# Optimization experiments

Hardware: AMD Instinct MI355X
Metric: run time of the kernel (lower is better)

## Reference

```python
import jax, jax.numpy as jnp
import numpy as np

N_NODES = 50000
N_EDGES = 1600000
IN_CH, OUT_CH, SIZE = 128, 64, 4


def _segment_softmax(e, seg, n):
    # numerically stable softmax of edge scores grouped by segment id (PyG softmax)
    m = jax.ops.segment_max(e, seg, num_segments=n)
    ex = jnp.exp(e - m[seg])
    s = jax.ops.segment_sum(ex, seg, num_segments=n)
    return ex / (s[seg] + 1e-16)


def setup_inputs() -> dict:
    key = jax.random.key(0)
    k = jax.random.split(key, 6)
    x = jax.random.normal(k[0], (N_NODES, IN_CH), dtype=jnp.float32)
    edge_index = jax.random.randint(k[1], (2, N_EDGES), 0, N_NODES, dtype=jnp.int64)
    W = jax.random.normal(k[2], (SIZE, IN_CH, OUT_CH), dtype=jnp.float32) * 0.1
    att_src = jax.random.normal(k[3], (SIZE, OUT_CH), dtype=jnp.float32) * 0.1
    att_dst = jax.random.normal(k[4], (SIZE, OUT_CH), dtype=jnp.float32) * 0.1
    bias = jnp.zeros((SIZE, OUT_CH), dtype=jnp.float32)
    return {"x": x, "W": W, "att_src": att_src, "att_dst": att_dst,
            "bias": bias, "edge_index": edge_index, "direction": 1}


def reference(x, W, att_src, att_dst, bias, edge_index, direction):
    src, dst = edge_index[0], edge_index[1]
    n = x.shape[0]
    size = W.shape[0]
    feat_sum = None
    att_sum = None
    for i in range(size):  # small fixed ensemble of GATConv layers
        h = x @ W[i]                                    # [N, out]
        a_s = h @ att_src[i]                            # [N] source scores
        a_d = h @ att_dst[i]                            # [N] target scores
        e = jax.nn.leaky_relu(a_s[src] + a_d[dst], 0.2)  # [E] GAT slope 0.2
        alpha = _segment_softmax(e, dst, n)             # softmax over incoming edges
        out = jax.ops.segment_sum(alpha[:, None] * h[src], dst, num_segments=n) + bias[i]
        fl = jax.nn.leaky_relu(out, 0.01)               # f.leaky_relu default slope
        feat_sum = fl if feat_sum is None else feat_sum + fl
        att_sum = alpha if att_sum is None else att_sum + alpha
    # directional node pooling: mean of summed edge attention grouped by source node
    counts = jax.ops.segment_sum(jnp.ones_like(att_sum), src, num_segments=n)
    pooled = jax.ops.segment_sum(att_sum, src, num_segments=n) / jnp.maximum(counts, 1.0)
    node_scores = direction * pooled
    return feat_sum, node_scores
```

## Files before the change

kernel.cpp:

```cpp
#include <hip/hip_runtime.h>
#include <stdint.h>

#define N_NODES 50000
#define N_EDGES 1600000
#define IN_CH   128
#define OUT_CH  64
#define CAP     72
#define NBUCKET 196
#define MB      782
#define NODES48 (MB * 64)
#define GB      3128
#define EPB2    2047
#define BK2     24
#define GOVF_CAP 8192
#define NODES_PAD (NBUCKET * 256)
#define SENTINEL 0xFFFFFFFFu

typedef float  f32x4  __attribute__((ext_vector_type(4)));
typedef __bf16 bf16x8 __attribute__((ext_vector_type(8)));

__device__ __forceinline__ unsigned int f2bf(float f) {
    unsigned int u = __float_as_uint(f);
    u += 0x7fffu + ((u >> 16) & 1u);
    return u >> 16;
}
__device__ __forceinline__ float lrelu(float v, float s) { return v > 0.f ? v : s * v; }

__device__ __forceinline__ void split2(float f, unsigned short& hi, unsigned short& lo) {
    unsigned int u = __float_as_uint(f);
    hi = (unsigned short)(u >> 16);
    float r = f - __uint_as_float(u & 0xffff0000u);
    lo = (unsigned short)f2bf(r);
}

#define POOL_SCALE 268435456.0f
#define POOL_MASK  ((1ull << 40) - 1ull)

__global__ __launch_bounds__(256) void k_prep(
    const float* __restrict__ W, const float* __restrict__ att_src,
    const float* __restrict__ att_dst,
    unsigned short* __restrict__ Wp,
    float* __restrict__ w_s, float* __restrict__ w_d, int* __restrict__ gcnt)
{
    __shared__ float sw[IN_CH * OUT_CH];
    const int l = blockIdx.x;
    const int tid = threadIdx.x;
    const float* Wb = W + (size_t)l * IN_CH * OUT_CH;

    for (int idx = tid; idx < IN_CH * OUT_CH; idx += 256) sw[idx] = Wb[idx];
    __syncthreads();

    for (int idx = tid; idx < 16 * 2 * 64; idx += 256) {
        int lane2 = idx & 63;
        int h2 = (idx >> 6) & 1;
        int f2 = idx >> 7;
        int ks = f2 >> 2, n = f2 & 3;
        int lg = lane2 >> 4, lr = lane2 & 15;
        unsigned short fr[8];
#pragma unroll
        for (int j = 0; j < 8; ++j) {
            int k = ks * 32 + lg * 8 + j;
            int c = n * 16 + lr;
            unsigned short hi, lo2;
            split2(sw[k * OUT_CH + c], hi, lo2);
            fr[j] = h2 ? lo2 : hi;
        }
        *(uint4*)(Wp + (((size_t)l * 16 + f2) * 2 + h2) * 512 + lane2 * 8) =
            *(const uint4*)fr;
    }
    if (tid < IN_CH) {
        float s = 0.f, d = 0.f;
        const float* As = att_src + l * OUT_CH;
        const float* Ad = att_dst + l * OUT_CH;
        const float* wr = sw + tid * OUT_CH;
#pragma unroll 8
        for (int c = 0; c < OUT_CH; ++c) { s = fmaf(wr[c], As[c], s); d = fmaf(wr[c], Ad[c], d); }
        w_s[l * IN_CH + tid] = s;
        w_d[l * IN_CH + tid] = d;
    }
    if (l == 0 && tid == 0) gcnt[0] = 0;
}

__global__ __launch_bounds__(256) void k_front(
    const float* __restrict__ x, const float* __restrict__ w_s,
    const float* __restrict__ w_d,
    unsigned int* __restrict__ X16, float* __restrict__ a_s, float* __restrict__ a_d,
    const int* __restrict__ ei, unsigned int* __restrict__ binned2,
    int* __restrict__ cnt2, int* __restrict__ gcnt, unsigned int* __restrict__ govf)
{
    __shared__ int lcnt[NBUCKET];
    __shared__ unsigned int stage[BK2 * 256];

    const int tid  = threadIdx.x;
    const int lane = tid & 63;
    const int q    = lane & 31;
    const int h    = lane >> 5;
    const int wv   = __builtin_amdgcn_readfirstlane(tid >> 6);
    const int blk  = blockIdx.x;
    const int row0 = blk * 64;

    {
        const float4* ws4 = (const float4*)w_s;
        const float4* wd4 = (const float4*)w_d;
        float4 rs0 = ws4[q], rs1 = ws4[32 + q], rs2 = ws4[64 + q], rs3 = ws4[96 + q];
        float4 rd0 = wd4[q], rd1 = wd4[32 + q], rd2 = wd4[64 + q], rd3 = wd4[96 + q];
#pragma unroll 2
        for (int r = 0; r < 8; ++r) {
            int node = row0 + wv * 16 + 2 * r + h;
            float4 xv = make_float4(0.f, 0.f, 0.f, 0.f);
            if (node < N_NODES)
                xv = ((const float4*)(x + (size_t)node * IN_CH))[q];
            if (node < N_NODES) {
                uint2 pk;
                pk.x = f2bf(xv.x) | (f2bf(xv.y) << 16);
                pk.y = f2bf(xv.z) | (f2bf(xv.w) << 16);
                ((uint2*)(X16 + (size_t)node * 64))[q] = pk;
            }
            float s0 = xv.x*rs0.x + xv.y*rs0.y + xv.z*rs0.z + xv.w*rs0.w;
            float s1 = xv.x*rs1.x + xv.y*rs1.y + xv.z*rs1.z + xv.w*rs1.w;
            float s2 = xv.x*rs2.x + xv.y*rs2.y + xv.z*rs2.z + xv.w*rs2.w;
            float s3 = xv.x*rs3.x + xv.y*rs3.y + xv.z*rs3.z + xv.w*rs3.w;
            float d0 = xv.x*rd0.x + xv.y*rd0.y + xv.z*rd0.z + xv.w*rd0.w;
            float d1 = xv.x*rd1.x + xv.y*rd1.y + xv.z*rd1.z + xv.w*rd1.w;
            float d2 = xv.x*rd2.x + xv.y*rd2.y + xv.z*rd2.z + xv.w*rd2.w;
            float d3 = xv.x*rd3.x + xv.y*rd3.y + xv.z*rd3.z + xv.w*rd3.w;
#pragma unroll
            for (int off = 1; off <= 16; off <<= 1) {
                s0 += __shfl_xor(s0, off); s1 += __shfl_xor(s1, off);
                s2 += __shfl_xor(s2, off); s3 += __shfl_xor(s3, off);
                d0 += __shfl_xor(d0, off); d1 += __shfl_xor(d1, off);
                d2 += __shfl_xor(d2, off); d3 += __shfl_xor(d3, off);
            }
            if (q == 0 && node < N_NODES) {
                ((float4*)a_s)[node] = make_float4(s0, s1, s2, s3);
                ((float4*)a_d)[node] = make_float4(d0, d1, d2, d3);
            }
        }
    }

    const int start = blk * EPB2;
    const int end = (start + EPB2 < N_EDGES) ? start + EPB2 : N_EDGES;

    int probe = ei[2 * (start + tid) + 1];
    const int is64 = (__ballot(probe != 0) == 0ull) ? 1 : 0;

    for (int i = tid; i < NBUCKET; i += 256) lcnt[i] = 0;
    __syncthreads();

    if (is64) {
        const int2* e2 = (const int2*)ei;
        for (int e = start + tid; e < end; e += 256) {
            int s = e2[e].x;
            int d = e2[(size_t)N_EDGES + e].x;
            int bk = d >> 8;
            unsigned int pk = ((unsigned int)s << 16) | (unsigned int)d;
            int pos = atomicAdd(&lcnt[bk], 1);
            if (pos < BK2) stage[pos * 256 + bk] = pk;
            else {
                int gi = atomicAdd(gcnt, 1);
                if (gi < GOVF_CAP) { govf[2 * gi] = (unsigned int)bk; govf[2 * gi + 1] = pk; }
            }
        }
    } else {
        for (int e = start + tid; e < end; e += 256) {
            int s = ei[e];
            int d = ei[N_EDGES + e];
            int bk = d >> 8;
            unsigned int pk = ((unsigned int)s << 16) | (unsigned int)d;
            int pos = atomicAdd(&lcnt[bk], 1);
            if (pos < BK2) stage[pos * 256 + bk] = pk;
            else {
                int gi = atomicAdd(gcnt, 1);
                if (gi < GOVF_CAP) { govf[2 * gi] = (unsigned int)bk; govf[2 * gi + 1] = pk; }
            }
        }
    }
    __syncthreads();

    if (tid < NBUCKET) {
        int c = lcnt[tid];
        if (c > BK2) c = BK2;
        cnt2[(size_t)tid * MB + blk] = c;
        uint4* dstp = (uint4*)(binned2 + ((size_t)tid * MB + blk) * BK2);
        for (int p = 0; p < c; p += 4) {
            uint4 v;
            v.x = stage[p * 256 + tid];
            v.y = (p + 1 < c) ? stage[(p + 1) * 256 + tid] : SENTINEL;
            v.z = (p + 2 < c) ? stage[(p + 2) * 256 + tid] : SENTINEL;
            v.w = (p + 3 < c) ? stage[(p + 3) * 256 + tid] : SENTINEL;
            dstp[p >> 2] = v;
        }
    }
}

__global__ __launch_bounds__(1024) void k_bucket(
    const unsigned int* __restrict__ binned2, const int* __restrict__ cnt2,
    const int* __restrict__ gcnt, const unsigned int* __restrict__ govf,
    unsigned short* __restrict__ slot, int* __restrict__ cnt_dst,
    unsigned long long* __restrict__ pool)
{
    __shared__ unsigned short sl[256 * CAP];
    __shared__ int cnt[256];
    const int b = blockIdx.x;
    const int tid = threadIdx.x;
    if (tid < 256) cnt[tid] = 0;
    int pidx = b * 1024 + tid;
    if (pidx < N_NODES) pool[pidx] = 0ull;
    __syncthreads();

    if (tid < MB) {
        int c = cnt2[(size_t)b * MB + tid];
        if (c > BK2) c = BK2;
        const uint4* cp = (const uint4*)(binned2 + ((size_t)b * MB + tid) * BK2);
        for (int p = 0; p < c; p += 4) {
            uint4 v = cp[p >> 2];
            {
                unsigned int pk = v.x; int local = pk & 255;
                int pos = atomicAdd(&cnt[local], 1);
                if (pos < CAP) sl[local * CAP + pos] = (unsigned short)(pk >> 16);
            }
            if (p + 1 < c) {
                unsigned int pk = v.y; int local = pk & 255;
                int pos = atomicAdd(&cnt[local], 1);
                if (pos < CAP) sl[local * CAP + pos] = (unsigned short)(pk >> 16);
            }
            if (p + 2 < c) {
                unsigned int pk = v.z; int local = pk & 255;
                int pos = atomicAdd(&cnt[local], 1);
                if (pos < CAP) sl[local * CAP + pos] = (unsigned short)(pk >> 16);
            }
            if (p + 3 < c) {
                unsigned int pk = v.w; int local = pk & 255;
                int pos = atomicAdd(&cnt[local], 1);
                if (pos < CAP) sl[local * CAP + pos] = (unsigned short)(pk >> 16);
            }
        }
    }
    {
        int nov = gcnt[0];
        if (nov > GOVF_CAP) nov = GOVF_CAP;
        for (int i = tid; i < nov; i += 1024) {
            if ((int)govf[2 * i] == b) {
                unsigned int pk = govf[2 * i + 1];
                int local = pk & 255;
                int pos = atomicAdd(&cnt[local], 1);
                if (pos < CAP) sl[local * CAP + pos] = (unsigned short)(pk >> 16);
            }
        }
    }
    __syncthreads();

    uint4* g = (uint4*)(slot + (size_t)b * 256 * CAP);
    const uint4* l = (const uint4*)sl;
    for (int i = tid; i < 256 * CAP * 2 / 16; i += 1024) g[i] = l[i];
    if (tid < 256) cnt_dst[b * 256 + tid] = cnt[tid];
}

__global__ __launch_bounds__(256) void k_gather(
    const unsigned int* __restrict__ X16, const unsigned short* __restrict__ slot,
    const int* __restrict__ cnt_dst,
    const float* __restrict__ a_s, const float* __restrict__ a_d,
    const unsigned short* __restrict__ Wp, const float* __restrict__ bias,
    unsigned long long* __restrict__ pool, float* __restrict__ out)
{
    __shared__ __align__(16) float ewlds[4][CAP * 4];
    __shared__ __align__(16) unsigned char smem[4 * 16 * 68 * 4];
    unsigned int* stageU = (unsigned int*)smem;
    float* red = (float*)smem;

    const int tid = threadIdx.x;
    const int lane = tid & 63;
    const int lr = lane & 15, lg = lane >> 4;
    const int wv = __builtin_amdgcn_readfirstlane(tid >> 6);
    const int blk = blockIdx.x;
    float* ewl = ewlds[wv];
    const float4* as4p = (const float4*)a_s;

#pragma unroll 1
    for (int sub = 0; sub < 4; ++sub) {
        const int t = wv * 4 + sub;
        const int node = blk * 16 + t;
        int deg = __builtin_amdgcn_readfirstlane(cnt_dst[node]);
        if (deg > CAP) deg = CAP;
        const unsigned short* s16 = slot + (size_t)node * CAP;
        const float4 ad4 = ((const float4*)a_d)[node];

        float se0 = 0.f, se1 = 0.f, se2 = 0.f, se3 = 0.f;
#pragma unroll
        for (int base = 0; base < CAP; base += 64) {
            int j = base + lane;
            if (j < deg) {
                int s = s16[j];
                float4 as4 = as4p[s];
                float t0 = as4.x + ad4.x, t1 = as4.y + ad4.y;
                float t2 = as4.z + ad4.z, t3 = as4.w + ad4.w;
                float4 e4;
                e4.x = __expf(fmaxf(t0, 0.2f * t0));
                e4.y = __expf(fmaxf(t1, 0.2f * t1));
                e4.z = __expf(fmaxf(t2, 0.2f * t2));
                e4.w = __expf(fmaxf(t3, 0.2f * t3));
                *(float4*)(ewl + j * 4) = e4;
                se0 += e4.x; se1 += e4.y; se2 += e4.z; se3 += e4.w;
            }
        }
#pragma unroll
        for (int off = 1; off <= 32; off <<= 1) {
            se0 += __shfl_xor(se0, off); se1 += __shfl_xor(se1, off);
            se2 += __shfl_xor(se2, off); se3 += __shfl_xor(se3, off);
        }
        const float i0 = 1.0f / (se0 + 1e-16f);
        const float i1 = 1.0f / (se1 + 1e-16f);
        const float i2 = 1.0f / (se2 + 1e-16f);
        const float i3 = 1.0f / (se3 + 1e-16f);

        float a00 = 0.f, a01 = 0.f, a10 = 0.f, a11 = 0.f;
        float a20 = 0.f, a21 = 0.f, a30 = 0.f, a31 = 0.f;
        const unsigned int* Xp = X16 + lane;

        auto body = [&](unsigned int s, int j) {
            float4 e4 = *(const float4*)(ewl + j * 4);
            unsigned int xv = Xp[(size_t)s * 64];
            float x0 = __uint_as_float(xv << 16);
            float x1 = __uint_as_float(xv & 0xffff0000u);
            a00 = fmaf(e4.x, x0, a00); a01 = fmaf(e4.x, x1, a01);
            a10 = fmaf(e4.y, x0, a10); a11 = fmaf(e4.y, x1, a11);
            a20 = fmaf(e4.z, x0, a20); a21 = fmaf(e4.z, x1, a21);
            a30 = fmaf(e4.w, x0, a30); a31 = fmaf(e4.w, x1, a31);
        };

        const unsigned int* sp = (const unsigned int*)s16;
        const int npair = deg >> 1;
        int j2 = 0;
        for (; j2 + 8 <= npair; j2 += 8) {
            uint4 pa = *(const uint4*)(sp + j2);
            uint4 pb = *(const uint4*)(sp + j2 + 4);
            body(pa.x & 0xffffu, 2*j2+0); body(pa.x >> 16, 2*j2+1);
            body(pa.y & 0xffffu, 2*j2+2); body(pa.y >> 16, 2*j2+3);
            body(pa.z & 0xffffu, 2*j2+4); body(pa.z >> 16, 2*j2+5);
            body(pa.w & 0xffffu, 2*j2+6); body(pa.w >> 16, 2*j2+7);
            body(pb.x & 0xffffu, 2*j2+8); body(pb.x >> 16, 2*j2+9);
            body(pb.y & 0xffffu, 2*j2+10); body(pb.y >> 16, 2*j2+11);
            body(pb.z & 0xffffu, 2*j2+12); body(pb.z >> 16, 2*j2+13);
            body(pb.w & 0xffffu, 2*j2+14); body(pb.w >> 16, 2*j2+15);
        }
        for (; j2 + 4 <= npair; j2 += 4) {
            uint4 p4 = *(const uint4*)(sp + j2);
            body(p4.x & 0xffffu, 2*j2+0); body(p4.x >> 16, 2*j2+1);
            body(p4.y & 0xffffu, 2*j2+2); body(p4.y >> 16, 2*j2+3);
            body(p4.z & 0xffffu, 2*j2+4); body(p4.z >> 16, 2*j2+5);
            body(p4.w & 0xffffu, 2*j2+6); body(p4.w >> 16, 2*j2+7);
        }
        for (; j2 < npair; ++j2) {
            unsigned int pr = sp[j2];
            body(pr & 0xffffu, 2*j2); body(pr >> 16, 2*j2+1);
        }
        if (deg & 1) body(sp[npair] & 0xffffu, deg - 1);

        {
            unsigned int swz = ((((unsigned)lane >> 2) ^ (unsigned)t) << 2) | (lane & 3);
            stageU[(t * 4 + 0) * 64 + swz] = f2bf(a00 * i0) | (f2bf(a01 * i0) << 16);
            stageU[(t * 4 + 1) * 64 + swz] = f2bf(a10 * i1) | (f2bf(a11 * i1) << 16);
            stageU[(t * 4 + 2) * 64 + swz] = f2bf(a20 * i2) | (f2bf(a21 * i2) << 16);
            stageU[(t * 4 + 3) * 64 + swz] = f2bf(a30 * i3) | (f2bf(a31 * i3) << 16);
        }

        for (int jj = lane; jj < deg; jj += 64) {
            int s = s16[jj];
            float4 e4 = *(const float4*)(ewl + jj * 4);
            float tot = e4.x * i0 + e4.y * i1 + e4.z * i2 + e4.w * i3;
            unsigned long long enc = (1ull << 40) |
                (unsigned long long)(tot * POOL_SCALE + 0.5f);
            atomicAdd(pool + s, enc);
        }
    }
    __syncthreads();

    const int l = wv;
    f32x4 acc[4];
#pragma unroll
    for (int n = 0; n < 4; ++n) acc[n] = (f32x4){0.f, 0.f, 0.f, 0.f};
#pragma unroll
    for (int ks = 0; ks < 4; ++ks) {
        int chunk = ((ks * 4 + lg) ^ lr) << 2;
        bf16x8 a = *(const bf16x8*)(stageU + (lr * 4 + l) * 64 + chunk);
#pragma unroll
        for (int n = 0; n < 4; ++n) {
            const unsigned short* fb =
                Wp + (((size_t)l * 16 + ks * 4 + n) * 2) * 512 + lane * 8;
            bf16x8 bhi = *(const bf16x8*)(fb);
            bf16x8 blo = *(const bf16x8*)(fb + 512);
            acc[n] = __builtin_amdgcn_mfma_f32_16x16x32_bf16(a, bhi, acc[n], 0, 0, 0);
            acc[n] = __builtin_amdgcn_mfma_f32_16x16x32_bf16(a, blo, acc[n], 0, 0, 0);
        }
    }
    __syncthreads();

#pragma unroll
    for (int n = 0; n < 4; ++n) {
        float bn = bias[l * OUT_CH + n * 16 + lr];
#pragma unroll
        for (int qq = 0; qq < 4; ++qq)
            red[(l * 16 + lg * 4 + qq) * 68 + n * 16 + lr] =
                lrelu(acc[n][qq] + bn, 0.01f);
    }
    __syncthreads();

    for (int i = tid; i < 16 * 64; i += 256) {
        int r = i >> 6, c = i & 63;
        int node = blk * 16 + r;
        if (node < N_NODES)
            out[(size_t)node * 64 + c] =
                red[(0 * 16 + r) * 68 + c] + red[(1 * 16 + r) * 68 + c] +
                red[(2 * 16 + r) * 68 + c] + red[(3 * 16 + r) * 68 + c];
    }
}

__global__ __launch_bounds__(256) void k_final(
    const unsigned long long* __restrict__ pool, const int* __restrict__ dirp,
    float* __restrict__ out)
{
    int i = blockIdx.x * 256 + threadIdx.x;
    if (i >= N_NODES) return;
    unsigned long long v = pool[i];
    unsigned int cnt = (unsigned int)(v >> 40);
    float val = (float)((double)(v & POOL_MASK) * (1.0 / (double)POOL_SCALE));
    int di = dirp[0];
    float dirf = (di >= -1000 && di <= 1000) ? (float)di : __int_as_float(di);
    float denom = (cnt > 1u) ? (float)cnt : 1.0f;
    out[(size_t)N_NODES * 64 + i] = dirf * val / denom;
}

extern "C" void kernel_launch(void* const* d_in, const int* in_sizes, int n_in,
                              void* d_out, int out_size, void* d_ws, size_t ws_size,
                              hipStream_t stream)
{
    const float* x       = (const float*)d_in[0];
    const float* W       = (const float*)d_in[1];
    const float* att_src = (const float*)d_in[2];
    const float* att_dst = (const float*)d_in[3];
    const float* bias    = (const float*)d_in[4];
    const int*   ei      = (const int*)d_in[5];
    const int*   dirp    = (const int*)d_in[6];
    float* out = (float*)d_out;

    char* w = (char*)d_ws;
    size_t off = 0;
    auto alloc = [&](size_t bytes) -> void* {
        void* p = w + off;
        off = (off + bytes + 255) & ~(size_t)255;
        return p;
    };
    unsigned long long* pool = (unsigned long long*)alloc((size_t)N_NODES * sizeof(unsigned long long));
    float* a_s = (float*)alloc((size_t)NODES48 * 4 * sizeof(float));
    float* a_d = (float*)alloc((size_t)NODES48 * 4 * sizeof(float));
    int* cnt_dst = (int*)alloc((size_t)NODES_PAD * sizeof(int));
    unsigned short* slot = (unsigned short*)alloc((size_t)NODES_PAD * CAP * sizeof(unsigned short));
    unsigned int* X16 = (unsigned int*)alloc((size_t)NODES48 * 64 * sizeof(unsigned int));
    unsigned short* Wp = (unsigned short*)alloc((size_t)4 * 16 * 2 * 512 * sizeof(unsigned short));
    float* w_s = (float*)alloc((size_t)4 * IN_CH * sizeof(float));
    float* w_d = (float*)alloc((size_t)4 * IN_CH * sizeof(float));
    int* cnt2 = (int*)alloc((size_t)NBUCKET * MB * sizeof(int));
    int* gcnt = (int*)alloc(256);
    unsigned int* govf = (unsigned int*)alloc((size_t)2 * GOVF_CAP * sizeof(unsigned int));
    unsigned int* binned2 = (unsigned int*)alloc((size_t)NBUCKET * MB * BK2 * sizeof(unsigned int));
    (void)ws_size; (void)in_sizes; (void)n_in; (void)out_size;

    k_prep<<<4, 256, 0, stream>>>(W, att_src, att_dst, Wp, w_s, w_d, gcnt);
    k_front<<<MB, 256, 0, stream>>>(x, w_s, w_d, X16, a_s, a_d, ei, binned2, cnt2,
                                    gcnt, govf);
    k_bucket<<<NBUCKET, 1024, 0, stream>>>(binned2, cnt2, gcnt, govf, slot, cnt_dst, pool);
    k_gather<<<GB, 256, 0, stream>>>(X16, slot, cnt_dst, a_s, a_d, Wp, bias, pool, out);
    k_final<<<(N_NODES + 255) / 256, 256, 0, stream>>>(pool, dirp, out);
}
```

Before: 233.8 us.

## Split front kernel roles across blocks and quarter the bucket kernel into smaller blocks

The front kernel now launches twice as many blocks. The first half converts x to bf16 and computes attention scores, and the second half bins edges, so the two phases run concurrently instead of serially within each block. The bucket kernel is split into four 256-thread blocks per bucket, each handling 64 destination nodes. That raises block count and cuts LDS per block, but every block rereads the whole bucket's binned edges and filters by quarter. The gather kernel also gets an occupancy hint of 8 blocks per SM, which may force register spills.

```diff
diff --git a/kernel.cpp b/kernel.cpp
--- a/kernel.cpp
+++ b/kernel.cpp
@@ -81,7 +81,7 @@
     if (l == 0 && tid == 0) gcnt[0] = 0;
 }
 
-__global__ __launch_bounds__(256) void k_front(
+__global__ __launch_bounds__(256) void k_combo(
     const float* __restrict__ x, const float* __restrict__ w_s,
     const float* __restrict__ w_d,
     unsigned int* __restrict__ X16, float* __restrict__ a_s, float* __restrict__ a_d,
@@ -96,10 +96,9 @@
     const int q    = lane & 31;
     const int h    = lane >> 5;
     const int wv   = __builtin_amdgcn_readfirstlane(tid >> 6);
-    const int blk  = blockIdx.x;
-    const int row0 = blk * 64;
-
-    {
+
+    if (blockIdx.x < MB) {
+        const int row0 = blockIdx.x * 64;
         const float4* ws4 = (const float4*)w_s;
         const float4* wd4 = (const float4*)w_d;
         float4 rs0 = ws4[q], rs1 = ws4[32 + q], rs2 = ws4[64 + q], rs3 = ws4[96 + q];
@@ -136,8 +135,10 @@
                 ((float4*)a_d)[node] = make_float4(d0, d1, d2, d3);
             }
         }
-    }
-
+        return;
+    }
+
+    const int blk = blockIdx.x - MB;
     const int start = blk * EPB2;
     const int end = (start + EPB2 < N_EDGES) ? start + EPB2 : N_EDGES;
 
@@ -193,70 +194,70 @@
     }
 }
 
-__global__ __launch_bounds__(1024) void k_bucket(
+__global__ __launch_bounds__(256) void k_bucket(
     const unsigned int* __restrict__ binned2, const int* __restrict__ cnt2,
     const int* __restrict__ gcnt, const unsigned int* __restrict__ govf,
     unsigned short* __restrict__ slot, int* __restrict__ cnt_dst,
     unsigned long long* __restrict__ pool)
 {
-    __shared__ unsigned short sl[256 * CAP];
-    __shared__ int cnt[256];
+    __shared__ unsigned short sl[64 * CAP];
+    __shared__ int cnt[64];
     const int b = blockIdx.x;
+    const int bucket = b >> 2;
+    const int quarter = b & 3;
     const int tid = threadIdx.x;
-    if (tid < 256) cnt[tid] = 0;
-    int pidx = b * 1024 + tid;
-    if (pidx < N_NODES) pool[pidx] = 0ull;
-    __syncthreads();
-
-    if (tid < MB) {
-        int c = cnt2[(size_t)b * MB + tid];
+    if (tid < 64) cnt[tid] = 0;
+    {
+        int pidx = b * 64 + tid;
+        if (tid < 64 && pidx < N_NODES) pool[pidx] = 0ull;
+    }
+    __syncthreads();
+
+    for (int cell = tid; cell < MB; cell += 256) {
+        int c = cnt2[(size_t)bucket * MB + cell];
         if (c > BK2) c = BK2;
-        const uint4* cp = (const uint4*)(binned2 + ((size_t)b * MB + tid) * BK2);
+        const uint4* cp = (const uint4*)(binned2 + ((size_t)bucket * MB + cell) * BK2);
         for (int p = 0; p < c; p += 4) {
             uint4 v = cp[p >> 2];
-            {
-                unsigned int pk = v.x; int local = pk & 255;
-                int pos = atomicAdd(&cnt[local], 1);
-                if (pos < CAP) sl[local * CAP + pos] = (unsigned short)(pk >> 16);
-            }
-            if (p + 1 < c) {
-                unsigned int pk = v.y; int local = pk & 255;
-                int pos = atomicAdd(&cnt[local], 1);
-                if (pos < CAP) sl[local * CAP + pos] = (unsigned short)(pk >> 16);
-            }
-            if (p + 2 < c) {
-                unsigned int pk = v.z; int local = pk & 255;
-                int pos = atomicAdd(&cnt[local], 1);
-                if (pos < CAP) sl[local * CAP + pos] = (unsigned short)(pk >> 16);
-            }
-            if (p + 3 < c) {
-                unsigned int pk = v.w; int local = pk & 255;
-                int pos = atomicAdd(&cnt[local], 1);
-                if (pos < CAP) sl[local * CAP + pos] = (unsigned short)(pk >> 16);
+            unsigned int pks[4] = {v.x, v.y, v.z, v.w};
+#pragma unroll
+            for (int u = 0; u < 4; ++u) {
+                if (p + u < c) {
+                    unsigned int pk = pks[u];
+                    int local = pk & 255;
+                    if ((local >> 6) == quarter) {
+                        int idx = local & 63;
+                        int pos = atomicAdd(&cnt[idx], 1);
+                        if (pos < CAP) sl[idx * CAP + pos] = (unsigned short)(pk >> 16);
+                    }
+                }
             }
         }
     }
     {
         int nov = gcnt[0];
         if (nov > GOVF_CAP) nov = GOVF_CAP;
-        for (int i = tid; i < nov; i += 1024) {
-            if ((int)govf[2 * i] == b) {
+        for (int i = tid; i < nov; i += 256) {
+            if ((int)govf[2 * i] == bucket) {
                 unsigned int pk = govf[2 * i + 1];
                 int local = pk & 255;
-                int pos = atomicAdd(&cnt[local], 1);
-                if (pos < CAP) sl[local * CAP + pos] = (unsigned short)(pk >> 16);
-            }
-        }
-    }
-    __syncthreads();
-
-    uint4* g = (uint4*)(slot + (size_t)b * 256 * CAP);
+                if ((local >> 6) == quarter) {
+                    int idx = local & 63;
+                    int pos = atomicAdd(&cnt[idx], 1);
+                    if (pos < CAP) sl[idx * CAP + pos] = (unsigned short)(pk >> 16);
+                }
+            }
+        }
+    }
+    __syncthreads();
+
+    uint4* g = (uint4*)(slot + (size_t)b * 64 * CAP);
     const uint4* l = (const uint4*)sl;
-    for (int i = tid; i < 256 * CAP * 2 / 16; i += 1024) g[i] = l[i];
-    if (tid < 256) cnt_dst[b * 256 + tid] = cnt[tid];
-}
-
-__global__ __launch_bounds__(256) void k_gather(
+    for (int i = tid; i < 64 * CAP * 2 / 16; i += 256) g[i] = l[i];
+    if (tid < 64) cnt_dst[b * 64 + tid] = cnt[tid];
+}
+
+__global__ __launch_bounds__(256, 8) void k_gather(
     const unsigned int* __restrict__ X16, const unsigned short* __restrict__ slot,
     const int* __restrict__ cnt_dst,
     const float* __restrict__ a_s, const float* __restrict__ a_d,
@@ -466,9 +467,9 @@
     (void)ws_size; (void)in_sizes; (void)n_in; (void)out_size;
 
     k_prep<<<4, 256, 0, stream>>>(W, att_src, att_dst, Wp, w_s, w_d, gcnt);
-    k_front<<<MB, 256, 0, stream>>>(x, w_s, w_d, X16, a_s, a_d, ei, binned2, cnt2,
-                                    gcnt, govf);
-    k_bucket<<<NBUCKET, 1024, 0, stream>>>(binned2, cnt2, gcnt, govf, slot, cnt_dst, pool);
+    k_combo<<<2 * MB, 256, 0, stream>>>(x, w_s, w_d, X16, a_s, a_d, ei, binned2, cnt2,
+                                        gcnt, govf);
+    k_bucket<<<4 * NBUCKET, 256, 0, stream>>>(binned2, cnt2, gcnt, govf, slot, cnt_dst, pool);
     k_gather<<<GB, 256, 0, stream>>>(X16, slot, cnt_dst, a_s, a_d, Wp, bias, pool, out);
     k_final<<<(N_NODES + 255) / 256, 256, 0, stream>>>(pool, dirp, out);
 }
```

After: 246.2 us. 1.05x slower.

## Two-pass windowed counting sort in bucket kernel, drop per-block count array

Applied to the files above, without the earlier changes.

The front kernel now pads every bucket chunk with sentinels to full length and stops writing a separate count array. The bucket kernel reads the whole padded region with coalesced flat loops in two passes. The first pass counts edges per destination and source-id window, and the second places source ids at prefix offsets, so each destination's neighbour list comes out roughly ordered by source. The aim is better locality for the gather kernel's source-feature loads and more parallel, coalesced reads in the bucket kernel. In exchange, binned2 is read twice, the full padded buffer is written and read, and shared-memory use grows.

```diff
diff --git a/kernel.cpp b/kernel.cpp
--- a/kernel.cpp
+++ b/kernel.cpp
@@ -86,7 +86,7 @@
     const float* __restrict__ w_d,
     unsigned int* __restrict__ X16, float* __restrict__ a_s, float* __restrict__ a_d,
     const int* __restrict__ ei, unsigned int* __restrict__ binned2,
-    int* __restrict__ cnt2, int* __restrict__ gcnt, unsigned int* __restrict__ govf)
+    int* __restrict__ gcnt, unsigned int* __restrict__ govf)
 {
     __shared__ int lcnt[NBUCKET];
     __shared__ unsigned int stage[BK2 * 256];
@@ -180,11 +180,10 @@
     if (tid < NBUCKET) {
         int c = lcnt[tid];
         if (c > BK2) c = BK2;
-        cnt2[(size_t)tid * MB + blk] = c;
         uint4* dstp = (uint4*)(binned2 + ((size_t)tid * MB + blk) * BK2);
-        for (int p = 0; p < c; p += 4) {
+        for (int p = 0; p < BK2; p += 4) {
             uint4 v;
-            v.x = stage[p * 256 + tid];
+            v.x = (p     < c) ? stage[p * 256 + tid]       : SENTINEL;
             v.y = (p + 1 < c) ? stage[(p + 1) * 256 + tid] : SENTINEL;
             v.z = (p + 2 < c) ? stage[(p + 2) * 256 + tid] : SENTINEL;
             v.w = (p + 3 < c) ? stage[(p + 3) * 256 + tid] : SENTINEL;
@@ -194,58 +193,73 @@
 }
 
 __global__ __launch_bounds__(1024) void k_bucket(
-    const unsigned int* __restrict__ binned2, const int* __restrict__ cnt2,
+    const unsigned int* __restrict__ binned2,
     const int* __restrict__ gcnt, const unsigned int* __restrict__ govf,
     unsigned short* __restrict__ slot, int* __restrict__ cnt_dst,
     unsigned long long* __restrict__ pool)
 {
     __shared__ unsigned short sl[256 * CAP];
-    __shared__ int cnt[256];
+    __shared__ int cnt8[256 * 8];
+    __shared__ int base8[256 * 8];
     const int b = blockIdx.x;
     const int tid = threadIdx.x;
-    if (tid < 256) cnt[tid] = 0;
-    int pidx = b * 1024 + tid;
-    if (pidx < N_NODES) pool[pidx] = 0ull;
-    __syncthreads();
-
-    if (tid < MB) {
-        int c = cnt2[(size_t)b * MB + tid];
-        if (c > BK2) c = BK2;
-        const uint4* cp = (const uint4*)(binned2 + ((size_t)b * MB + tid) * BK2);
-        for (int p = 0; p < c; p += 4) {
-            uint4 v = cp[p >> 2];
-            {
-                unsigned int pk = v.x; int local = pk & 255;
-                int pos = atomicAdd(&cnt[local], 1);
-                if (pos < CAP) sl[local * CAP + pos] = (unsigned short)(pk >> 16);
-            }
-            if (p + 1 < c) {
-                unsigned int pk = v.y; int local = pk & 255;
-                int pos = atomicAdd(&cnt[local], 1);
-                if (pos < CAP) sl[local * CAP + pos] = (unsigned short)(pk >> 16);
-            }
-            if (p + 2 < c) {
-                unsigned int pk = v.z; int local = pk & 255;
-                int pos = atomicAdd(&cnt[local], 1);
-                if (pos < CAP) sl[local * CAP + pos] = (unsigned short)(pk >> 16);
-            }
-            if (p + 3 < c) {
-                unsigned int pk = v.w; int local = pk & 255;
-                int pos = atomicAdd(&cnt[local], 1);
-                if (pos < CAP) sl[local * CAP + pos] = (unsigned short)(pk >> 16);
-            }
-        }
-    }
+    for (int i = tid; i < 256 * 8; i += 1024) cnt8[i] = 0;
     {
-        int nov = gcnt[0];
-        if (nov > GOVF_CAP) nov = GOVF_CAP;
-        for (int i = tid; i < nov; i += 1024) {
-            if ((int)govf[2 * i] == b) {
-                unsigned int pk = govf[2 * i + 1];
-                int local = pk & 255;
-                int pos = atomicAdd(&cnt[local], 1);
-                if (pos < CAP) sl[local * CAP + pos] = (unsigned short)(pk >> 16);
-            }
+        int pidx = b * 1024 + tid;
+        if (pidx < N_NODES) pool[pidx] = 0ull;
+    }
+    __syncthreads();
+
+    const int total = MB * BK2;
+    const unsigned int* src = binned2 + (size_t)b * total;
+    int nov = gcnt[0];
+    if (nov > GOVF_CAP) nov = GOVF_CAP;
+
+    for (int i = tid; i < total; i += 1024) {
+        unsigned int p = src[i];
+        if (p == SENTINEL) continue;
+        int local = p & 255;
+        int win = (p >> 16) >> 13;
+        atomicAdd(&cnt8[local * 8 + win], 1);
+    }
+    for (int i = tid; i < nov; i += 1024) {
+        if ((int)govf[2 * i] == b) {
+            unsigned int pk = govf[2 * i + 1];
+            atomicAdd(&cnt8[(pk & 255) * 8 + ((pk >> 16) >> 13)], 1);
+        }
+    }
+    __syncthreads();
+
+    if (tid < 256) {
+        int s = 0;
+#pragma unroll
+        for (int w = 0; w < 8; ++w) {
+            base8[tid * 8 + w] = s;
+            s += cnt8[tid * 8 + w];
+        }
+        cnt_dst[b * 256 + tid] = s;
+#pragma unroll
+        for (int w = 0; w < 8; ++w) cnt8[tid * 8 + w] = 0;
+    }
+    __syncthreads();
+
+    for (int i = tid; i < total; i += 1024) {
+        unsigned int p = src[i];
+        if (p == SENTINEL) continue;
+        int local = p & 255;
+        unsigned int s = p >> 16;
+        int win = s >> 13;
+        int pos = base8[local * 8 + win] + atomicAdd(&cnt8[local * 8 + win], 1);
+        if (pos < CAP) sl[local * CAP + pos] = (unsigned short)s;
+    }
+    for (int i = tid; i < nov; i += 1024) {
+        if ((int)govf[2 * i] == b) {
+            unsigned int pk = govf[2 * i + 1];
+            int local = pk & 255;
+            unsigned int s = pk >> 16;
+            int win = s >> 13;
+            int pos = base8[local * 8 + win] + atomicAdd(&cnt8[local * 8 + win], 1);
+            if (pos < CAP) sl[local * CAP + pos] = (unsigned short)s;
         }
     }
     __syncthreads();
@@ -253,7 +267,6 @@
     uint4* g = (uint4*)(slot + (size_t)b * 256 * CAP);
     const uint4* l = (const uint4*)sl;
     for (int i = tid; i < 256 * CAP * 2 / 16; i += 1024) g[i] = l[i];
-    if (tid < 256) cnt_dst[b * 256 + tid] = cnt[tid];
 }
 
 __global__ __launch_bounds__(256) void k_gather(
@@ -459,16 +472,15 @@
     unsigned short* Wp = (unsigned short*)alloc((size_t)4 * 16 * 2 * 512 * sizeof(unsigned short));
     float* w_s = (float*)alloc((size_t)4 * IN_CH * sizeof(float));
     float* w_d = (float*)alloc((size_t)4 * IN_CH * sizeof(float));
-    int* cnt2 = (int*)alloc((size_t)NBUCKET * MB * sizeof(int));
     int* gcnt = (int*)alloc(256);
     unsigned int* govf = (unsigned int*)alloc((size_t)2 * GOVF_CAP * sizeof(unsigned int));
     unsigned int* binned2 = (unsigned int*)alloc((size_t)NBUCKET * MB * BK2 * sizeof(unsigned int));
     (void)ws_size; (void)in_sizes; (void)n_in; (void)out_size;
 
     k_prep<<<4, 256, 0, stream>>>(W, att_src, att_dst, Wp, w_s, w_d, gcnt);
-    k_front<<<MB, 256, 0, stream>>>(x, w_s, w_d, X16, a_s, a_d, ei, binned2, cnt2,
+    k_front<<<MB, 256, 0, stream>>>(x, w_s, w_d, X16, a_s, a_d, ei, binned2,
                                     gcnt, govf);
-    k_bucket<<<NBUCKET, 1024, 0, stream>>>(binned2, cnt2, gcnt, govf, slot, cnt_dst, pool);
+    k_bucket<<<NBUCKET, 1024, 0, stream>>>(binned2, gcnt, govf, slot, cnt_dst, pool);
     k_gather<<<GB, 256, 0, stream>>>(X16, slot, cnt_dst, a_s, a_d, Wp, bias, pool, out);
     k_final<<<(N_NODES + 255) / 256, 256, 0, stream>>>(pool, dirp, out);
 }
```

New measurement: 236.9 us. About the same (+1.3%).
